# Kernel optimization log

Hardware: AMD Instinct MI355X
Metric: run time of the kernel (lower is better)

## Reference

```python
import jax, jax.numpy as jnp
import numpy as np

B, T, HIN = 4, 2048, 1024
H, E = 16, 64


def setup_inputs() -> dict:
    key = jax.random.key(0)
    k1, k2, k3, k4, k5 = jax.random.split(key, 5)
    s = 1.0 / np.sqrt(HIN)
    return {
        "query": jax.random.normal(k1, (B, T, HIN), dtype=jnp.float32),
        "key_value": jax.random.normal(k2, (B, T, HIN), dtype=jnp.float32),
        "Wq": jax.random.uniform(k3, (HIN, H * E), dtype=jnp.float32, minval=-s, maxval=s),
        "Wk": jax.random.uniform(k4, (HIN, H * E), dtype=jnp.float32, minval=-s, maxval=s),
        "Wv": jax.random.uniform(k5, (HIN, H * E), dtype=jnp.float32, minval=-s, maxval=s),
    }


def reference(query, key_value, Wq, Wk, Wv):
    b, t, _ = query.shape
    scale = E ** (-0.25)  # applied to both q and k, matching e**(1/4) division
    q = (query @ Wq).reshape(b, t, H, E) * scale      # [b,t,h,e]
    k = (key_value @ Wk).reshape(b, t, H, E) * scale  # [b,t,h,e]
    v = (key_value @ Wv).reshape(b, t, H, E)          # [b,t,h,e]
    dot = jnp.einsum("bqhe,bkhe->bhqk", q, k)         # [b,h,t,t]
    attn = jax.nn.softmax(dot, axis=-1)
    out = jnp.einsum("bhqk,bkhe->bqhe", attn, v)      # [b,t,h,e]
    return out.reshape(b, t, H * E)
```

## Files before the change

### kernel.cpp

```cpp
#include <hip/hip_runtime.h>
#include <hip/hip_bf16.h>
#include <stdint.h>


typedef __bf16 bf16;
typedef __attribute__((ext_vector_type(8))) __bf16 bf16x8;
typedef __attribute__((ext_vector_type(4))) __bf16 bf16x4;
typedef __attribute__((ext_vector_type(4))) float f32x4;
typedef __attribute__((ext_vector_type(4))) short s16x4;

#define B_    4
#define T_    2048
#define HIN_  1024
#define H_    16
#define E_    64
#define NOUT_ 1024
#define LOG2E 1.4426950408889634f
#define QKSCALE 0.35355339059327373f
#define QSCALE  (QKSCALE * LOG2E)

__device__ __forceinline__ void gl_lds16(const void* g, void* l) {
  __builtin_amdgcn_global_load_lds((__attribute__((address_space(1))) void*)g,
                                   (__attribute__((address_space(3))) void*)l,
                                   16, 0, 0);
}

__global__ __launch_bounds__(256) void cvt_kernel(const float* __restrict__ Xq,
                                                  const float* __restrict__ Xkv,
                                                  bf16* __restrict__ Xb) {
  const float* src = blockIdx.y ? Xkv : Xq;
  bf16* dst = Xb + (size_t)blockIdx.y * (8192 * 1024);
  size_t i = ((size_t)blockIdx.x * 256 + threadIdx.x) * 8;
  float4 f0 = ((const float4*)(src + i))[0];
  float4 f1 = ((const float4*)(src + i))[1];
  bf16x8 t = {(bf16)f0.x, (bf16)f0.y, (bf16)f0.z, (bf16)f0.w,
              (bf16)f1.x, (bf16)f1.y, (bf16)f1.z, (bf16)f1.w};
  *(bf16x8*)(dst + i) = t;
}

__global__ __launch_bounds__(256) void wt_kernel(const float* __restrict__ Wq,
                                                 const float* __restrict__ Wk,
                                                 const float* __restrict__ Wv,
                                                 bf16* __restrict__ Wt) {
  __shared__ float s[32][33];
  const int z = blockIdx.z;
  const float* W = (z == 0) ? Wq : ((z == 1) ? Wk : Wv);
  bf16* out = Wt + (size_t)z * HIN_ * NOUT_;
  const int n0 = blockIdx.x * 32, k0 = blockIdx.y * 32;
  const int tx = threadIdx.x, ty = threadIdx.y;
#pragma unroll
  for (int i = 0; i < 4; i++)
    s[ty + i * 8][tx] = W[(size_t)(k0 + ty + i * 8) * NOUT_ + n0 + tx];
  __syncthreads();
#pragma unroll
  for (int i = 0; i < 4; i++)
    out[(size_t)(n0 + ty + i * 8) * HIN_ + k0 + tx] = (bf16)s[tx][ty + i * 8];
}

__global__ __launch_bounds__(256, 4) void proj_kernel(const bf16* __restrict__ Xb,
                                                      const bf16* __restrict__ Wt,
                                                      bf16* __restrict__ Qb,
                                                      bf16* __restrict__ Kb,
                                                      bf16* __restrict__ Vtb) {
  __shared__ bf16 As[128 * 64];
  __shared__ bf16 Bs[128 * 64];
  const int z = blockIdx.z;
  const bf16* Abase = (z == 0) ? Xb : ((z == 1) ? Xb + (size_t)8192 * 1024 : Wt + (size_t)2 * HIN_ * NOUT_);
  const bf16* Bbase = (z == 0) ? Wt : ((z == 1) ? Wt + (size_t)HIN_ * NOUT_ : Xb + (size_t)8192 * 1024);
  const int mt = (z == 2) ? blockIdx.y : blockIdx.x;
  const int nt = (z == 2) ? blockIdx.x : blockIdx.y;
  const int m0 = mt * 128, n0 = nt * 128;
  const int tid = threadIdx.x;
  const int w = tid >> 6, lane = tid & 63, quad = lane >> 4, lo = lane & 15;
  const int wm = (w >> 1) * 64, wn = (w & 1) * 64;
  const int srow = w * 8 + (lane >> 3);
  const int schunk = (lane & 7) ^ (srow & 7);

  f32x4 acc[4][4] = {};

  for (int k0 = 0; k0 < HIN_; k0 += 64) {
    __syncthreads();
#pragma unroll
    for (int j = 0; j < 4; j++) {
      int row = j * 32 + srow;
      gl_lds16(Abase + (size_t)(m0 + row) * HIN_ + k0 + schunk * 8, As + (j * 32 + w * 8) * 64);
      gl_lds16(Bbase + (size_t)(n0 + row) * HIN_ + k0 + schunk * 8, Bs + (j * 32 + w * 8) * 64);
    }
    __syncthreads();
#pragma unroll
    for (int kk = 0; kk < 2; kk++) {
      bf16x8 bfrag[4], afrag[4];
#pragma unroll
      for (int j = 0; j < 4; j++) {
        int off = ((((kk << 2) + quad) ^ (lo & 7)) << 3);
        bfrag[j] = *(const bf16x8*)(Bs + (wn + j * 16 + lo) * 64 + off);
        afrag[j] = *(const bf16x8*)(As + (wm + j * 16 + lo) * 64 + off);
      }
#pragma unroll
      for (int i = 0; i < 4; i++)
#pragma unroll
        for (int j = 0; j < 4; j++)
          acc[i][j] = __builtin_amdgcn_mfma_f32_16x16x32_bf16(afrag[i], bfrag[j], acc[i][j], 0, 0, 0);
    }
  }

#pragma unroll
  for (int i = 0; i < 4; i++)
#pragma unroll
    for (int j = 0; j < 4; j++)
#pragma unroll
      for (int r = 0; r < 4; r++) {
        int m = m0 + wm + i * 16 + quad * 4 + r;
        int n = n0 + wn + j * 16 + lo;
        float v = acc[i][j][r];
        if (z == 2) {
          int h = m >> 6, e = m & 63, b = n >> 11, t = n & 2047;
          Vtb[(((size_t)b * H_ + h) * E_ + e) * T_ + t] = (bf16)v;
        } else {
          int b = m >> 11, t = m & 2047, h = n >> 6, e = n & 63;
          if (z == 0)
            Qb[(((size_t)b * H_ + h) * T_ + t) * E_ + e] = (bf16)(v * QSCALE);
          else
            Kb[(((size_t)b * H_ + h) * T_ + t) * E_ + e] = (bf16)(v * QKSCALE);
        }
      }
}

__global__ __launch_bounds__(128, 2) void attn_kernel(const bf16* __restrict__ Qb,
                                                      const bf16* __restrict__ Kb,
                                                      const bf16* __restrict__ Vtb,
                                                      float* __restrict__ out) {
  __shared__ bf16 Ks[64 * 64];
  __shared__ bf16 Vts[64 * 64];
  const int tid = threadIdx.x;
  const int w = tid >> 6, lane = tid & 63, quad = lane >> 4, lo = lane & 15;
  const int bh = blockIdx.x, q0 = blockIdx.y * 128;
  const int wq = q0 + w * 64;
  const bf16* Qg = Qb + (size_t)bh * T_ * E_;
  const bf16* Kg = Kb + (size_t)bh * T_ * E_;
  const bf16* Vg = Vtb + (size_t)bh * E_ * T_;
  const int srow = lane >> 3;
  const int schunk = (lane & 7) ^ (srow & 7);

  bf16x8 qf[4][2];
#pragma unroll
  for (int qi = 0; qi < 4; qi++)
#pragma unroll
    for (int ks = 0; ks < 2; ks++)
      qf[qi][ks] = *(const bf16x8*)(Qg + (size_t)(wq + qi * 16 + lo) * E_ + ks * 32 + quad * 8);

  f32x4 acc[4][4] = {};
  float lsum[4] = {0.f, 0.f, 0.f, 0.f};

  for (int kt = 0; kt < T_ / 64; kt++) {
    __syncthreads();
#pragma unroll
    for (int i = 0; i < 4; i++) {
      int row = w * 32 + i * 8 + srow;
      gl_lds16(Kg + (size_t)(kt * 64 + row) * E_ + schunk * 8, Ks + (w * 32 + i * 8) * 64);
      gl_lds16(Vg + (size_t)row * T_ + kt * 64 + schunk * 8, Vts + (w * 32 + i * 8) * 64);
    }
    __syncthreads();

    bf16x8 kf[4][2];
#pragma unroll
    for (int ti = 0; ti < 4; ti++)
#pragma unroll
      for (int ks = 0; ks < 2; ks++)
        kf[ti][ks] = *(const bf16x8*)(Ks + (ti * 16 + lo) * 64 + ((((ks << 2) + quad) ^ (lo & 7)) << 3));

    bf16x4 pf[4][4];
#pragma unroll
    for (int qi = 0; qi < 4; qi++) {
      f32x4 st[4] = {};
#pragma unroll
      for (int ks = 0; ks < 2; ks++)
#pragma unroll
        for (int ti = 0; ti < 4; ti++)
          st[ti] = __builtin_amdgcn_mfma_f32_16x16x32_bf16(kf[ti][ks], qf[qi][ks], st[ti], 0, 0, 0);
      float ls = 0.f;
#pragma unroll
      for (int ti = 0; ti < 4; ti++) {
        bf16x4 p4;
#pragma unroll
        for (int r = 0; r < 4; r++) {
          float p = __builtin_amdgcn_exp2f(st[ti][r]);
          ls += p;
          p4[r] = (bf16)p;
        }
        pf[qi][ti] = p4;
      }
      lsum[qi] += ls;
    }

#pragma unroll
    for (int tc = 0; tc < 4; tc++)
#pragma unroll
      for (int ej = 0; ej < 4; ej++) {
        bf16x4 vf = *(const bf16x4*)(Vts + (ej * 16 + lo) * 64 +
                                     (((tc * 2 + (quad >> 1)) ^ (lo & 7)) << 3) + (quad & 1) * 4);
#pragma unroll
        for (int qi = 0; qi < 4; qi++)
          acc[qi][ej] = __builtin_amdgcn_mfma_f32_16x16x16bf16_1k(
              __builtin_bit_cast(s16x4, pf[qi][tc]), __builtin_bit_cast(s16x4, vf),
              acc[qi][ej], 0, 0, 0);
      }
  }

  const int b = bh >> 4, h = bh & 15;
#pragma unroll
  for (int qi = 0; qi < 4; qi++) {
    float l = lsum[qi];
    l += __shfl_xor(l, 16);
    l += __shfl_xor(l, 32);
#pragma unroll
    for (int r = 0; r < 4; r++) {
      float linv = __builtin_amdgcn_rcpf(__shfl(l, quad * 4 + r));
      size_t t = q0 + w * 64 + qi * 16 + quad * 4 + r;
#pragma unroll
      for (int ej = 0; ej < 4; ej++)
        out[((size_t)b * T_ + t) * NOUT_ + h * E_ + ej * 16 + lo] = acc[qi][ej][r] * linv;
    }
  }
}

extern "C" void kernel_launch(void* const* d_in, const int* in_sizes, int n_in,
                              void* d_out, int out_size, void* d_ws, size_t ws_size,
                              hipStream_t stream) {
  const float* Xq  = (const float*)d_in[0];
  const float* Xkv = (const float*)d_in[1];
  const float* Wq  = (const float*)d_in[2];
  const float* Wk  = (const float*)d_in[3];
  const float* Wv  = (const float*)d_in[4];
  float* out = (float*)d_out;

  char* ws = (char*)d_ws;
  bf16* Qb  = (bf16*)(ws);
  bf16* Kb  = (bf16*)(ws + ((size_t)16 << 20));
  bf16* Vtb = (bf16*)(ws + ((size_t)32 << 20));
  bf16* Wt  = (bf16*)(ws + ((size_t)48 << 20));
  bf16* Xb  = (bf16*)d_out;

  hipLaunchKernelGGL(cvt_kernel, dim3(4096, 2), dim3(256), 0, stream, Xq, Xkv, Xb);
  hipLaunchKernelGGL(wt_kernel, dim3(32, 32, 3), dim3(32, 8), 0, stream, Wq, Wk, Wv, Wt);
  hipLaunchKernelGGL(proj_kernel, dim3(64, 8, 3), dim3(256), 0, stream, Xb, Wt, Qb, Kb, Vtb);
  hipLaunchKernelGGL(attn_kernel, dim3(64, 16), dim3(128), 0, stream, Qb, Kb, Vtb, out);
}
```

Baseline: 260.7 us.

## Merge prep kernels, double-buffer projection GEMM, compute softmax sum via MFMA

Three separate changes. The activation conversion and weight transpose kernels become one launch, saving a kernel launch and its tail. The projection GEMM gets double-buffered LDS, so the next K tile's global-to-LDS loads are issued before computing on the current one. In attention, the per-row softmax denominator is accumulated with an extra MFMA against a ones vector instead of scalar adds and cross-lane shuffles; this adds MFMA work but removes VALU adds. The GEMM pipeline has only one barrier per iteration, so the loads into the next buffer may race with slower waves still reading it, which is a correctness risk. Doubling the LDS buffers may also lower occupancy.

Measured after the change: 272.8 us. 1.05x slower.

```diff
diff --git a/kernel.cpp b/kernel.cpp
--- a/kernel.cpp
+++ b/kernel.cpp
@@ -25,36 +25,39 @@
                                    16, 0, 0);
 }
 
-__global__ __launch_bounds__(256) void cvt_kernel(const float* __restrict__ Xq,
-                                                  const float* __restrict__ Xkv,
-                                                  bf16* __restrict__ Xb) {
-  const float* src = blockIdx.y ? Xkv : Xq;
-  bf16* dst = Xb + (size_t)blockIdx.y * (8192 * 1024);
-  size_t i = ((size_t)blockIdx.x * 256 + threadIdx.x) * 8;
-  float4 f0 = ((const float4*)(src + i))[0];
-  float4 f1 = ((const float4*)(src + i))[1];
-  bf16x8 t = {(bf16)f0.x, (bf16)f0.y, (bf16)f0.z, (bf16)f0.w,
-              (bf16)f1.x, (bf16)f1.y, (bf16)f1.z, (bf16)f1.w};
-  *(bf16x8*)(dst + i) = t;
-}
-
-__global__ __launch_bounds__(256) void wt_kernel(const float* __restrict__ Wq,
-                                                 const float* __restrict__ Wk,
-                                                 const float* __restrict__ Wv,
-                                                 bf16* __restrict__ Wt) {
+__global__ __launch_bounds__(256) void prep_kernel(const float* __restrict__ Xq,
+                                                   const float* __restrict__ Xkv,
+                                                   const float* __restrict__ Wq,
+                                                   const float* __restrict__ Wk,
+                                                   const float* __restrict__ Wv,
+                                                   bf16* __restrict__ Xb,
+                                                   bf16* __restrict__ Wt) {
   __shared__ float s[32][33];
-  const int z = blockIdx.z;
-  const float* W = (z == 0) ? Wq : ((z == 1) ? Wk : Wv);
-  bf16* out = Wt + (size_t)z * HIN_ * NOUT_;
-  const int n0 = blockIdx.x * 32, k0 = blockIdx.y * 32;
-  const int tx = threadIdx.x, ty = threadIdx.y;
-#pragma unroll
-  for (int i = 0; i < 4; i++)
-    s[ty + i * 8][tx] = W[(size_t)(k0 + ty + i * 8) * NOUT_ + n0 + tx];
-  __syncthreads();
-#pragma unroll
-  for (int i = 0; i < 4; i++)
-    out[(size_t)(n0 + ty + i * 8) * HIN_ + k0 + tx] = (bf16)s[tx][ty + i * 8];
+  const int bid = blockIdx.x, tid = threadIdx.x;
+  if (bid < 8192) {
+    const float* src = (bid < 4096) ? Xq : Xkv;
+    bf16* dst = Xb + (size_t)(bid >> 12) * (8192 * 1024);
+    size_t i = ((size_t)(bid & 4095) * 256 + tid) * 8;
+    float4 f0 = ((const float4*)(src + i))[0];
+    float4 f1 = ((const float4*)(src + i))[1];
+    bf16x8 t = {(bf16)f0.x, (bf16)f0.y, (bf16)f0.z, (bf16)f0.w,
+                (bf16)f1.x, (bf16)f1.y, (bf16)f1.z, (bf16)f1.w};
+    *(bf16x8*)(dst + i) = t;
+  } else {
+    const int wb = bid - 8192;
+    const int z = wb >> 10, r = wb & 1023;
+    const float* W = (z == 0) ? Wq : ((z == 1) ? Wk : Wv);
+    bf16* out = Wt + (size_t)z * HIN_ * NOUT_;
+    const int n0 = (r & 31) * 32, k0 = (r >> 5) * 32;
+    const int tx = tid & 31, ty = tid >> 5;
+#pragma unroll
+    for (int i = 0; i < 4; i++)
+      s[ty + i * 8][tx] = W[(size_t)(k0 + ty + i * 8) * NOUT_ + n0 + tx];
+    __syncthreads();
+#pragma unroll
+    for (int i = 0; i < 4; i++)
+      out[(size_t)(n0 + ty + i * 8) * HIN_ + k0 + tx] = (bf16)s[tx][ty + i * 8];
+  }
 }
 
 __global__ __launch_bounds__(256, 4) void proj_kernel(const bf16* __restrict__ Xb,
@@ -62,8 +65,8 @@
                                                       bf16* __restrict__ Qb,
                                                       bf16* __restrict__ Kb,
                                                       bf16* __restrict__ Vtb) {
-  __shared__ bf16 As[128 * 64];
-  __shared__ bf16 Bs[128 * 64];
+  __shared__ bf16 As[2][128 * 64];
+  __shared__ bf16 Bs[2][128 * 64];
   const int z = blockIdx.z;
   const bf16* Abase = (z == 0) ? Xb : ((z == 1) ? Xb + (size_t)8192 * 1024 : Wt + (size_t)2 * HIN_ * NOUT_);
   const bf16* Bbase = (z == 0) ? Wt : ((z == 1) ? Wt + (size_t)HIN_ * NOUT_ : Xb + (size_t)8192 * 1024);
@@ -78,23 +81,31 @@
 
   f32x4 acc[4][4] = {};
 
-  for (int k0 = 0; k0 < HIN_; k0 += 64) {
-    __syncthreads();
+#pragma unroll
+  for (int j = 0; j < 4; j++) {
+    int row = j * 32 + srow;
+    gl_lds16(Abase + (size_t)(m0 + row) * HIN_ + schunk * 8, &As[0][(j * 32 + w * 8) * 64]);
+    gl_lds16(Bbase + (size_t)(n0 + row) * HIN_ + schunk * 8, &Bs[0][(j * 32 + w * 8) * 64]);
+  }
+
+  for (int kb = 0; kb < 16; kb++) {
+    const int cur = kb & 1, nxt = cur ^ 1;
+    __syncthreads();
+    const int kn = ((kb + 1) & 15) * 64;
 #pragma unroll
     for (int j = 0; j < 4; j++) {
       int row = j * 32 + srow;
-      gl_lds16(Abase + (size_t)(m0 + row) * HIN_ + k0 + schunk * 8, As + (j * 32 + w * 8) * 64);
-      gl_lds16(Bbase + (size_t)(n0 + row) * HIN_ + k0 + schunk * 8, Bs + (j * 32 + w * 8) * 64);
-    }
-    __syncthreads();
+      gl_lds16(Abase + (size_t)(m0 + row) * HIN_ + kn + schunk * 8, &As[nxt][(j * 32 + w * 8) * 64]);
+      gl_lds16(Bbase + (size_t)(n0 + row) * HIN_ + kn + schunk * 8, &Bs[nxt][(j * 32 + w * 8) * 64]);
+    }
 #pragma unroll
     for (int kk = 0; kk < 2; kk++) {
       bf16x8 bfrag[4], afrag[4];
 #pragma unroll
       for (int j = 0; j < 4; j++) {
         int off = ((((kk << 2) + quad) ^ (lo & 7)) << 3);
-        bfrag[j] = *(const bf16x8*)(Bs + (wn + j * 16 + lo) * 64 + off);
-        afrag[j] = *(const bf16x8*)(As + (wm + j * 16 + lo) * 64 + off);
+        bfrag[j] = *(const bf16x8*)(&Bs[cur][(wn + j * 16 + lo) * 64 + off]);
+        afrag[j] = *(const bf16x8*)(&As[cur][(wm + j * 16 + lo) * 64 + off]);
       }
 #pragma unroll
       for (int i = 0; i < 4; i++)
@@ -149,8 +160,12 @@
     for (int ks = 0; ks < 2; ks++)
       qf[qi][ks] = *(const bf16x8*)(Qg + (size_t)(wq + qi * 16 + lo) * E_ + ks * 32 + quad * 8);
 
+  const bf16 one = (bf16)1.0f;
+  const bf16x4 ones4 = {one, one, one, one};
+  const s16x4 onesf = __builtin_bit_cast(s16x4, ones4);
+
   f32x4 acc[4][4] = {};
-  float lsum[4] = {0.f, 0.f, 0.f, 0.f};
+  f32x4 acc_l[4] = {};
 
   for (int kt = 0; kt < T_ / 64; kt++) {
     __syncthreads();
@@ -178,23 +193,18 @@
 #pragma unroll
         for (int ti = 0; ti < 4; ti++)
           st[ti] = __builtin_amdgcn_mfma_f32_16x16x32_bf16(kf[ti][ks], qf[qi][ks], st[ti], 0, 0, 0);
-      float ls = 0.f;
 #pragma unroll
       for (int ti = 0; ti < 4; ti++) {
         bf16x4 p4;
 #pragma unroll
-        for (int r = 0; r < 4; r++) {
-          float p = __builtin_amdgcn_exp2f(st[ti][r]);
-          ls += p;
-          p4[r] = (bf16)p;
-        }
+        for (int r = 0; r < 4; r++)
+          p4[r] = (bf16)__builtin_amdgcn_exp2f(st[ti][r]);
         pf[qi][ti] = p4;
       }
-      lsum[qi] += ls;
-    }
-
-#pragma unroll
-    for (int tc = 0; tc < 4; tc++)
+    }
+
+#pragma unroll
+    for (int tc = 0; tc < 4; tc++) {
 #pragma unroll
       for (int ej = 0; ej < 4; ej++) {
         bf16x4 vf = *(const bf16x4*)(Vts + (ej * 16 + lo) * 64 +
@@ -205,23 +215,24 @@
               __builtin_bit_cast(s16x4, pf[qi][tc]), __builtin_bit_cast(s16x4, vf),
               acc[qi][ej], 0, 0, 0);
       }
+#pragma unroll
+      for (int qi = 0; qi < 4; qi++)
+        acc_l[qi] = __builtin_amdgcn_mfma_f32_16x16x16bf16_1k(
+            __builtin_bit_cast(s16x4, pf[qi][tc]), onesf, acc_l[qi], 0, 0, 0);
+    }
   }
 
   const int b = bh >> 4, h = bh & 15;
 #pragma unroll
-  for (int qi = 0; qi < 4; qi++) {
-    float l = lsum[qi];
-    l += __shfl_xor(l, 16);
-    l += __shfl_xor(l, 32);
+  for (int qi = 0; qi < 4; qi++)
 #pragma unroll
     for (int r = 0; r < 4; r++) {
-      float linv = __builtin_amdgcn_rcpf(__shfl(l, quad * 4 + r));
-      size_t t = q0 + w * 64 + qi * 16 + quad * 4 + r;
+      float linv = __builtin_amdgcn_rcpf(acc_l[qi][r]);
+      size_t t = wq + qi * 16 + quad * 4 + r;
 #pragma unroll
       for (int ej = 0; ej < 4; ej++)
         out[((size_t)b * T_ + t) * NOUT_ + h * E_ + ej * 16 + lo] = acc[qi][ej][r] * linv;
     }
-  }
 }
 
 extern "C" void kernel_launch(void* const* d_in, const int* in_sizes, int n_in,
@@ -241,8 +252,7 @@
   bf16* Wt  = (bf16*)(ws + ((size_t)48 << 20));
   bf16* Xb  = (bf16*)d_out;
 
-  hipLaunchKernelGGL(cvt_kernel, dim3(4096, 2), dim3(256), 0, stream, Xq, Xkv, Xb);
-  hipLaunchKernelGGL(wt_kernel, dim3(32, 32, 3), dim3(32, 8), 0, stream, Wq, Wk, Wv, Wt);
+  hipLaunchKernelGGL(prep_kernel, dim3(11264), dim3(256), 0, stream, Xq, Xkv, Wq, Wk, Wv, Xb, Wt);
   hipLaunchKernelGGL(proj_kernel, dim3(64, 8, 3), dim3(256), 0, stream, Xb, Wt, Qb, Kb, Vtb);
   hipLaunchKernelGGL(attn_kernel, dim3(64, 16), dim3(128), 0, stream, Qb, Kb, Vtb, out);
 }
```
